# Performance work log

Hardware: AMD Instinct MI355X
Metric: run time of the kernel (lower is better)

The kernel has to match this reference:

```python
import jax, jax.numpy as jnp
import numpy as np

B, S, H, NH = 2, 2048, 2048, 16
DH = H // NH


def setup_inputs() -> dict:
    key = jax.random.key(0)
    ks = jax.random.split(key, 9)
    scale = 1.0 / np.sqrt(H)
    inp = {
        "hidden_state": jax.random.normal(ks[0], (B, S, H), dtype=jnp.float32),
        "Wq": jax.random.normal(ks[1], (H, H), dtype=jnp.float32) * scale,
        "bq": jnp.zeros((H,), dtype=jnp.float32),
        "Wk": jax.random.normal(ks[2], (H, H), dtype=jnp.float32) * scale,
        "bk": jnp.zeros((H,), dtype=jnp.float32),
        "Wv": jax.random.normal(ks[3], (H, H), dtype=jnp.float32) * scale,
        "bv": jnp.zeros((H,), dtype=jnp.float32),
        "Wo": jax.random.normal(ks[4], (H, H), dtype=jnp.float32) * scale,
        "bo": jnp.zeros((H,), dtype=jnp.float32),
    }
    # additive causal mask: 0 on/below diagonal, large negative above
    neg = jnp.float32(-1e9)
    tri = jnp.tril(jnp.ones((S, S), dtype=bool))
    inp["causal_mask"] = jnp.where(tri, 0.0, neg)[None, None, :, :]
    return inp


def reference(hidden_state, Wq, bq, Wk, bk, Wv, bv, Wo, bo, causal_mask):
    def split_heads(x):  # [B,S,H] -> [B,NH,S,DH]
        return x.reshape(B, S, NH, DH).transpose(0, 2, 1, 3)

    q = split_heads(hidden_state @ Wq + bq)
    k = split_heads(hidden_state @ Wk + bk)
    v = split_heads(hidden_state @ Wv + bv)

    scores = jnp.einsum("bhqd,bhkd->bhqk", q, k) / jnp.sqrt(jnp.float32(DH))
    scores = scores + causal_mask
    probs = jax.nn.softmax(scores, axis=-1)
    out = jnp.einsum("bhqk,bhkd->bhqd", probs, v)  # [B,NH,S,DH]
    out = out.transpose(0, 2, 1, 3).reshape(B, S, H)
    return out @ Wo + bo
```

## Files before the change

kernel.cpp:

```cpp
#include <hip/hip_runtime.h>
#include <cstdint>

typedef __attribute__((ext_vector_type(4))) float f32x4;
typedef __attribute__((ext_vector_type(16))) float f32x16;
typedef __attribute__((ext_vector_type(8))) __bf16 bf16x8;
typedef __attribute__((ext_vector_type(4))) unsigned short u16x4;
typedef __attribute__((ext_vector_type(2))) unsigned int u32x2;
typedef __attribute__((ext_vector_type(4))) float fvec4;

#define DEV __device__ __forceinline__
#define MFMA16(a, b, c) __builtin_amdgcn_mfma_f32_16x16x32_bf16((a), (b), (c), 0, 0, 0)
#define MFMA32(a, b, c) __builtin_amdgcn_mfma_f32_32x32x16_bf16((a), (b), (c), 0, 0, 0)

DEV unsigned short f2bf(float f) {
  union { float f; uint32_t u; } c; c.f = f;
  uint32_t u = c.u;
  return (unsigned short)((u + 0x7FFFu + ((u >> 16) & 1u)) >> 16);
}

DEV unsigned int pack2(float lo, float hi) {
  union { float f; uint32_t u; } a, b;
  a.f = lo; b.f = hi;
  return __builtin_amdgcn_perm(b.u + 0x8000u, a.u + 0x8000u, 0x07060302u);
}

DEV void gll16(const void* g, void* l) {
  __builtin_amdgcn_global_load_lds(
      (const __attribute__((address_space(1))) void*)(uintptr_t)g,
      (__attribute__((address_space(3))) void*)(uint32_t)(uintptr_t)l,
      16, 0, 0);
}

__global__ void cvt_bf16(const float* __restrict__ src, unsigned short* __restrict__ dst) {
  int i = (blockIdx.x * 256 + threadIdx.x) * 4;
  fvec4 v = *(const fvec4*)(src + i);
  u16x4 o;
  o[0] = f2bf(v[0]); o[1] = f2bf(v[1]); o[2] = f2bf(v[2]); o[3] = f2bf(v[3]);
  *(u16x4*)(dst + i) = o;
}

__global__ void transpose_cvt4(const float* __restrict__ W0, const float* __restrict__ W1,
                               const float* __restrict__ W2, const float* __restrict__ W3,
                               unsigned short* __restrict__ Dqkv, unsigned short* __restrict__ Do) {
  __shared__ float t[32][33];
  const float* W = blockIdx.z == 0 ? W0 : blockIdx.z == 1 ? W1 : blockIdx.z == 2 ? W2 : W3;
  unsigned short* WT = blockIdx.z < 3 ? Dqkv + (size_t)blockIdx.z * 2048 * 2048 : Do;
  int n0 = blockIdx.x * 32, k0 = blockIdx.y * 32;
  int x = threadIdx.x, y = threadIdx.y;
  #pragma unroll
  for (int i = 0; i < 32; i += 8)
    t[y + i][x] = W[(size_t)(k0 + y + i) * 2048 + n0 + x];
  __syncthreads();
  #pragma unroll
  for (int i = 0; i < 32; i += 8)
    WT[(size_t)(n0 + y + i) * 2048 + k0 + x] = f2bf(t[x][y + i]);
}

constexpr float QSC = 0.08838834764831845f * 1.4426950408889634f;

template <int MODE>
__global__ __launch_bounds__(256, 2) void gemm128(
    const unsigned short* __restrict__ A,
    const unsigned short* __restrict__ Bt,
    const float* __restrict__ b0, const float* __restrict__ b1,
    const float* __restrict__ b2,
    void* __restrict__ o0, void* __restrict__ o1, void* __restrict__ o2) {
  __shared__ unsigned short As[128 * 64];
  __shared__ unsigned short Bs[128 * 64];
  const int id = blockIdx.x;
  const int m0 = (((id & 7) << 2) | ((id >> 3) & 3)) * 128;
  const int n0 = (id >> 5) * 128;
  const int tid = threadIdx.x;
  const int wave = tid >> 6, lid = tid & 63;
  const int l16 = lid & 15, lq = lid >> 4;
  const int wm = (wave >> 1) * 64, wn = (wave & 1) * 64;

  const int srow = lid >> 3;
  const int sgrp = (lid & 7) ^ srow;

  f32x4 acc[4][4] = {};

  for (int k0 = 0; k0 < 2048; k0 += 64) {
    #pragma unroll
    for (int i = 0; i < 4; ++i) {
      const int t = wave * 4 + i;
      const int r = t * 8 + srow;
      gll16(A + (size_t)(m0 + r) * 2048 + k0 + sgrp * 8, (char*)As + t * 1024 + lid * 16);
      gll16(Bt + (size_t)(n0 + r) * 2048 + k0 + sgrp * 8, (char*)Bs + t * 1024 + lid * 16);
    }
    __syncthreads();
    #pragma unroll
    for (int kk = 0; kk < 2; ++kk) {
      const int G = kk * 4 + lq;
      bf16x8 af[4], bfr[4];
      #pragma unroll
      for (int i = 0; i < 4; ++i)
        af[i] = *(const bf16x8*)(As + (wm + i * 16 + l16) * 64 + ((G ^ (l16 & 7)) << 3));
      #pragma unroll
      for (int j = 0; j < 4; ++j)
        bfr[j] = *(const bf16x8*)(Bs + (wn + j * 16 + l16) * 64 + ((G ^ (l16 & 7)) << 3));
      #pragma unroll
      for (int i = 0; i < 4; ++i)
        #pragma unroll
        for (int j = 0; j < 4; ++j)
          acc[i][j] = MFMA16(af[i], bfr[j], acc[i][j]);
    }
    __syncthreads();
  }

  #pragma unroll
  for (int j = 0; j < 4; ++j) {
    const int c = n0 + wn + j * 16 + l16;
    if (MODE == 1) {
      const int which = c >> 11;
      const int hd = c & 2047;
      const int h = hd >> 7, d = hd & 127;
      const float* bp = which == 0 ? b0 : which == 1 ? b1 : b2;
      const float bv = bp[hd];
      if (which == 2) {
        #pragma unroll
        for (int i = 0; i < 4; ++i) {
          const int row0 = m0 + wm + i * 16 + lq * 4;
          const int bb = row0 >> 11, s0 = row0 & 2047;
          u16x4 pv;
          #pragma unroll
          for (int r = 0; r < 4; ++r) pv[r] = f2bf(acc[i][j][r] + bv);
          *(u16x4*)((unsigned short*)o2 + ((size_t)((bb * 16 + h) * 128 + d)) * 2048 + s0) = pv;
        }
      } else {
        const float sc = which == 0 ? QSC : 1.0f;
        unsigned short* op = which == 0 ? (unsigned short*)o0 : (unsigned short*)o1;
        #pragma unroll
        for (int i = 0; i < 4; ++i) {
          #pragma unroll
          for (int r = 0; r < 4; ++r) {
            const int row = m0 + wm + i * 16 + lq * 4 + r;
            const int bb = row >> 11, s = row & 2047;
            op[(size_t)((bb * 16 + h) * 2048 + s) * 128 + d] = f2bf((acc[i][j][r] + bv) * sc);
          }
        }
      }
    } else {
      const float bv = b0[c];
      #pragma unroll
      for (int i = 0; i < 4; ++i)
        #pragma unroll
        for (int r = 0; r < 4; ++r) {
          const int row = m0 + wm + i * 16 + lq * 4 + r;
          ((float*)o0)[(size_t)row * 2048 + c] = acc[i][j][r] + bv;
        }
    }
  }
}

__global__ __launch_bounds__(256, 2) void attn(
    const unsigned short* __restrict__ Q,
    const unsigned short* __restrict__ K,
    const unsigned short* __restrict__ Vt,
    unsigned short* __restrict__ ctx) {
  __shared__ unsigned short Ks[64 * 128];
  __shared__ unsigned short Vts[128 * 64];
  __shared__ unsigned short Ps[4 * 32 * 64];

  const int bh = blockIdx.y;
  const int jq = (bh < 16) ? (15 - (int)blockIdx.x) : (int)blockIdx.x;
  const int q0 = jq * 128;
  const int b = bh >> 4, h = bh & 15;
  const unsigned short* Qh = Q + (size_t)bh * 2048 * 128;
  const unsigned short* Kh = K + (size_t)bh * 2048 * 128;
  const unsigned short* Vth = Vt + (size_t)bh * 128 * 2048;

  const int tid = threadIdx.x;
  const int wave = tid >> 6, lid = tid & 63;
  const int l32 = lid & 31, half = lid >> 5;
  const int qrow = q0 + wave * 32 + l32;
  unsigned short* Pw = Ps + wave * 2048 + l32 * 64;
  const int qsw = l32 & 7;

  bf16x8 qf[8];
  #pragma unroll
  for (int ds = 0; ds < 8; ++ds)
    qf[ds] = *(const bf16x8*)(Qh + (size_t)qrow * 128 + ds * 16 + half * 8);

  float m_i = -1e30f, l_i = 0.f;
  f32x16 acc[4] = {};

  const int ntiles = 2 * jq + 2;
  for (int jt = 0; jt < ntiles; ++jt) {
    const int k0 = jt * 64;
    #pragma unroll
    for (int ii = 0; ii < 4; ++ii) {
      const int t = wave * 4 + ii;
      const int r = t * 4 + (lid >> 4);
      const int g = (lid & 15) ^ (r & 15);
      gll16(Kh + (size_t)(k0 + r) * 128 + g * 8, (char*)Ks + t * 1024 + lid * 16);
    }
    #pragma unroll
    for (int ii = 0; ii < 4; ++ii) {
      const int t = wave * 4 + ii;
      const int d = t * 8 + (lid >> 3);
      const int g = (lid & 7) ^ (d & 7);
      gll16(Vth + (size_t)d * 2048 + k0 + g * 8, (char*)Vts + t * 1024 + lid * 16);
    }
    __syncthreads();

    f32x16 sacc[2] = {};
    #pragma unroll
    for (int ds = 0; ds < 8; ++ds) {
      #pragma unroll
      for (int mb = 0; mb < 2; ++mb) {
        const int kr = mb * 32 + l32;
        bf16x8 af = *(const bf16x8*)(Ks + kr * 128 + (((ds * 2 + half) ^ (kr & 15)) << 3));
        sacc[mb] = MFMA32(af, qf[ds], sacc[mb]);
      }
    }

    if (jt >= 2 * jq) {
      #pragma unroll
      for (int mb = 0; mb < 2; ++mb)
        #pragma unroll
        for (int i = 0; i < 16; ++i) {
          const int kg = k0 + mb * 32 + (i & 3) + 8 * (i >> 2) + 4 * half;
          if (kg > qrow) sacc[mb][i] = -1e30f;
        }
    }

    float tmax = -1e30f;
    #pragma unroll
    for (int mb = 0; mb < 2; ++mb)
      #pragma unroll
      for (int i = 0; i < 16; ++i) tmax = fmaxf(tmax, sacc[mb][i]);
    tmax = fmaxf(tmax, __shfl_xor(tmax, 32));

    const float mnew = fmaxf(m_i, tmax);
    const float alpha = exp2f(m_i - mnew);
    m_i = mnew;

    float ps = 0.f;
    #pragma unroll
    for (int mb = 0; mb < 2; ++mb) {
      #pragma unroll
      for (int i = 0; i < 16; ++i) {
        sacc[mb][i] = exp2f(sacc[mb][i] - mnew);
        ps += sacc[mb][i];
      }
      #pragma unroll
      for (int u = 0; u < 4; ++u) {
        u32x2 w;
        w[0] = pack2(sacc[mb][4 * u], sacc[mb][4 * u + 1]);
        w[1] = pack2(sacc[mb][4 * u + 2], sacc[mb][4 * u + 3]);
        *(u32x2*)(Pw + (((u + mb * 4) ^ qsw) << 3) + half * 4) = w;
      }
    }
    ps += __shfl_xor(ps, 32);
    l_i = l_i * alpha + ps;
    #pragma unroll
    for (int db = 0; db < 4; ++db)
      #pragma unroll
      for (int i = 0; i < 16; ++i) acc[db][i] *= alpha;

    #pragma unroll
    for (int ks = 0; ks < 4; ++ks) {
      bf16x8 pf = *(const bf16x8*)(Pw + (((ks * 2 + half) ^ qsw) << 3));
      #pragma unroll
      for (int db = 0; db < 4; ++db) {
        const int d = db * 32 + l32;
        bf16x8 vf = *(const bf16x8*)(Vts + d * 64 + (((ks * 2 + half) ^ (d & 7)) << 3));
        acc[db] = MFMA32(vf, pf, acc[db]);
      }
    }
    __syncthreads();
  }

  const float inv = 1.f / l_i;
  const size_t base = ((size_t)(b * 2048 + qrow)) * 2048 + h * 128;
  #pragma unroll
  for (int db = 0; db < 4; ++db) {
    #pragma unroll
    for (int u = 0; u < 4; ++u) {
      u32x2 w;
      w[0] = pack2(acc[db][4 * u] * inv, acc[db][4 * u + 1] * inv);
      w[1] = pack2(acc[db][4 * u + 2] * inv, acc[db][4 * u + 3] * inv);
      *(u32x2*)(ctx + base + db * 32 + 8 * u + 4 * half) = w;
    }
  }
}

extern "C" void kernel_launch(void* const* d_in, const int* in_sizes, int n_in,
                              void* d_out, int out_size, void* d_ws, size_t ws_size,
                              hipStream_t stream) {
  const float* hs = (const float*)d_in[0];
  const float* Wq = (const float*)d_in[1];
  const float* bq = (const float*)d_in[2];
  const float* Wk = (const float*)d_in[3];
  const float* bk = (const float*)d_in[4];
  const float* Wv = (const float*)d_in[5];
  const float* bv = (const float*)d_in[6];
  const float* Wo = (const float*)d_in[7];
  const float* bo = (const float*)d_in[8];
  float* out = (float*)d_out;

  char* ws = (char*)d_ws;
  unsigned short* hsb   = (unsigned short*)(ws);
  unsigned short* wqkvt = (unsigned short*)(ws + (16 << 20));
  unsigned short* wot   = (unsigned short*)(ws + (40 << 20));
  unsigned short* Qb    = (unsigned short*)(ws + (48 << 20));
  unsigned short* Kb    = (unsigned short*)(ws + (64 << 20));
  unsigned short* Vtb   = (unsigned short*)(ws + (80 << 20));
  unsigned short* ctx   = (unsigned short*)(ws + (96 << 20));

  cvt_bf16<<<dim3(8192), dim3(256), 0, stream>>>(hs, hsb);
  transpose_cvt4<<<dim3(64, 64, 4), dim3(32, 8), 0, stream>>>(Wq, Wk, Wv, Wo, wqkvt, wot);

  gemm128<1><<<dim3(1536), 256, 0, stream>>>(hsb, wqkvt, bq, bk, bv,
                                             (void*)Qb, (void*)Kb, (void*)Vtb);
  attn<<<dim3(16, 32), 256, 0, stream>>>(Qb, Kb, Vtb, ctx);
  gemm128<0><<<dim3(512), 256, 0, stream>>>(ctx, wot, bo, nullptr, nullptr,
                                            (void*)out, nullptr, nullptr);
}
```

Before: 392.3 us.

## Replace QKV projection GEMM with 256x256-tile, 8-wave pipelined kernel

The fused QKV projection now runs in a new kernel that computes 256x256 output tiles with 512 threads. It double-buffers LDS through direct global-to-LDS loads, interleaved across eight sub-phases per pair of K-steps. The kernel uses explicit barriers, waitcnt, sched_barrier and setprio around MFMA clusters, and an XCD-aware block remap. The aim is to raise arithmetic intensity and overlap memory with compute, at the cost of heavy register and LDS use (128 KB shared). The old gemm128 mode-1 epilogue is removed, leaving the template serving only the output projection.

```diff
diff --git a/kernel.cpp b/kernel.cpp
--- a/kernel.cpp
+++ b/kernel.cpp
@@ -111,43 +111,139 @@
   #pragma unroll
   for (int j = 0; j < 4; ++j) {
     const int c = n0 + wn + j * 16 + l16;
-    if (MODE == 1) {
-      const int which = c >> 11;
-      const int hd = c & 2047;
-      const int h = hd >> 7, d = hd & 127;
-      const float* bp = which == 0 ? b0 : which == 1 ? b1 : b2;
-      const float bv = bp[hd];
-      if (which == 2) {
+    const float bv = b0[c];
+    #pragma unroll
+    for (int i = 0; i < 4; ++i)
+      #pragma unroll
+      for (int r = 0; r < 4; ++r) {
+        const int row = m0 + wm + i * 16 + lq * 4 + r;
+        ((float*)o0)[(size_t)row * 2048 + c] = acc[i][j][r] + bv;
+      }
+  }
+}
+
+#define STA(c, kt, q) do { \
+  _Pragma("unroll") for (int jj = 0; jj < 2; ++jj) { \
+    const int j = (q) + jj * 2; \
+    const int r = j * 64 + srow; \
+    const int g = schk ^ (r & 7); \
+    gll16(A + (size_t)(m0 + r) * 2048 + ((kt) << 6) + g * 8, \
+          (char*)Als + (c) * 32768 + j * 8192 + tid * 16); \
+  } } while (0)
+
+#define STB(c, kt, q) do { \
+  _Pragma("unroll") for (int jj = 0; jj < 2; ++jj) { \
+    const int j = (q) * 2 + jj; \
+    const int L = j * 64 + srow; \
+    const int n = (((L & 127) >> 5) << 6) + ((L >> 7) << 5) + (L & 31); \
+    const int g = schk ^ (L & 7); \
+    gll16(Bt + (size_t)(n0 + n) * 2048 + ((kt) << 6) + g * 8, \
+          (char*)Bls + (c) * 32768 + j * 8192 + tid * 16); \
+  } } while (0)
+
+#define PHASE(CUR, QM, QN, STAGE, VM) do { \
+  bf16x8 af[4][2], bf_[2][2]; \
+  const unsigned short* Ab = Als + (CUR) * 16384; \
+  const unsigned short* Bb = Bls + (CUR) * 16384; \
+  _Pragma("unroll") for (int m = 0; m < 4; ++m) { \
+    const int row = wr * 128 + ((QM) * 4 + m) * 16 + l16; \
+    _Pragma("unroll") for (int kk = 0; kk < 2; ++kk) \
+      af[m][kk] = *(const bf16x8*)(Ab + row * 64 + (((kk * 4 + lq) ^ (row & 7)) << 3)); \
+  } \
+  _Pragma("unroll") for (int n = 0; n < 2; ++n) { \
+    const int bg = wc * 64 + ((QN) * 2 + n) * 16 + l16; \
+    const int L = (((bg >> 5) & 1) << 7) | ((bg >> 6) << 5) | (bg & 31); \
+    _Pragma("unroll") for (int kk = 0; kk < 2; ++kk) \
+      bf_[n][kk] = *(const bf16x8*)(Bb + L * 64 + (((kk * 4 + lq) ^ (L & 7)) << 3)); \
+  } \
+  STAGE; \
+  __builtin_amdgcn_sched_barrier(0); \
+  __builtin_amdgcn_s_barrier(); \
+  asm volatile("s_waitcnt lgkmcnt(0)" ::: "memory"); \
+  __builtin_amdgcn_sched_barrier(0); \
+  __builtin_amdgcn_s_setprio(1); \
+  _Pragma("unroll") for (int m = 0; m < 4; ++m) \
+    _Pragma("unroll") for (int n = 0; n < 2; ++n) \
+      _Pragma("unroll") for (int kk = 0; kk < 2; ++kk) \
+        acc[(QM) * 4 + m][(QN) * 2 + n] = \
+            MFMA16(af[m][kk], bf_[n][kk], acc[(QM) * 4 + m][(QN) * 2 + n]); \
+  __builtin_amdgcn_s_setprio(0); \
+  __builtin_amdgcn_sched_barrier(0); \
+  VM; \
+  __builtin_amdgcn_s_barrier(); \
+} while (0)
+
+__global__ __launch_bounds__(512, 2) void gemm256qkv(
+    const unsigned short* __restrict__ A,
+    const unsigned short* __restrict__ Bt,
+    const float* __restrict__ b0, const float* __restrict__ b1,
+    const float* __restrict__ b2,
+    unsigned short* __restrict__ oQ, unsigned short* __restrict__ oK,
+    unsigned short* __restrict__ oV) {
+  __shared__ unsigned short Als[32768];
+  __shared__ unsigned short Bls[32768];
+
+  const int id = blockIdx.x;
+  const int wg = (id & 7) * 48 + (id >> 3);
+  const int mt = wg / 24, nt = wg % 24;
+  const int m0 = mt << 8, n0 = nt << 8;
+
+  const int tid = threadIdx.x;
+  const int wave = tid >> 6, lid = tid & 63;
+  const int l16 = lid & 15, lq = lid >> 4;
+  const int wr = wave >> 2, wc = wave & 3;
+  const int srow = tid >> 3;
+  const int schk = tid & 7;
+
+  f32x4 acc[8][4] = {};
+
+  STA(0, 0, 0); STA(0, 0, 1); STB(0, 0, 0); STB(0, 0, 1);
+  STA(1, 1, 0); STB(1, 1, 0);
+  asm volatile("s_waitcnt vmcnt(4)" ::: "memory");
+  __builtin_amdgcn_s_barrier();
+
+  #pragma unroll 1
+  for (int i = 0; i < 16; ++i) {
+    const int t1 = 2 * i + 1;
+    const int t2 = (2 * i + 2 < 32) ? 2 * i + 2 : 31;
+    const int t3 = (2 * i + 3 < 32) ? 2 * i + 3 : 31;
+    PHASE(0, 0, 0, { STA(1, t1, 1); STB(1, t1, 1); }, );
+    PHASE(0, 0, 1, , );
+    PHASE(0, 1, 0, STA(0, t2, 0), );
+    PHASE(0, 1, 1, STB(0, t2, 0), asm volatile("s_waitcnt vmcnt(4)" ::: "memory"));
+    PHASE(1, 0, 0, { STA(0, t2, 1); STB(0, t2, 1); }, );
+    PHASE(1, 0, 1, , );
+    PHASE(1, 1, 0, STA(1, t3, 0), );
+    PHASE(1, 1, 1, STB(1, t3, 0), asm volatile("s_waitcnt vmcnt(4)" ::: "memory"));
+  }
+
+  const int which = n0 >> 11;
+  const float* bp = which == 0 ? b0 : which == 1 ? b1 : b2;
+  #pragma unroll
+  for (int n = 0; n < 4; ++n) {
+    const int hd = (n0 & 2047) + wc * 64 + n * 16 + l16;
+    const int h = hd >> 7, d = hd & 127;
+    const float bv = bp[hd];
+    if (which == 2) {
+      #pragma unroll
+      for (int m = 0; m < 8; ++m) {
+        const int row0 = m0 + wr * 128 + m * 16 + lq * 4;
+        const int bb = row0 >> 11, s0 = row0 & 2047;
+        u16x4 pv;
         #pragma unroll
-        for (int i = 0; i < 4; ++i) {
-          const int row0 = m0 + wm + i * 16 + lq * 4;
-          const int bb = row0 >> 11, s0 = row0 & 2047;
-          u16x4 pv;
-          #pragma unroll
-          for (int r = 0; r < 4; ++r) pv[r] = f2bf(acc[i][j][r] + bv);
-          *(u16x4*)((unsigned short*)o2 + ((size_t)((bb * 16 + h) * 128 + d)) * 2048 + s0) = pv;
-        }
-      } else {
-        const float sc = which == 0 ? QSC : 1.0f;
-        unsigned short* op = which == 0 ? (unsigned short*)o0 : (unsigned short*)o1;
-        #pragma unroll
-        for (int i = 0; i < 4; ++i) {
-          #pragma unroll
-          for (int r = 0; r < 4; ++r) {
-            const int row = m0 + wm + i * 16 + lq * 4 + r;
-            const int bb = row >> 11, s = row & 2047;
-            op[(size_t)((bb * 16 + h) * 2048 + s) * 128 + d] = f2bf((acc[i][j][r] + bv) * sc);
-          }
-        }
+        for (int r = 0; r < 4; ++r) pv[r] = f2bf(acc[m][n][r] + bv);
+        *(u16x4*)(oV + ((size_t)((bb * 16 + h) * 128 + d)) * 2048 + s0) = pv;
       }
     } else {
-      const float bv = b0[c];
-      #pragma unroll
-      for (int i = 0; i < 4; ++i)
+      const float sc = which == 0 ? QSC : 1.0f;
+      unsigned short* op = which == 0 ? oQ : oK;
+      #pragma unroll
+      for (int m = 0; m < 8; ++m)
         #pragma unroll
         for (int r = 0; r < 4; ++r) {
-          const int row = m0 + wm + i * 16 + lq * 4 + r;
-          ((float*)o0)[(size_t)row * 2048 + c] = acc[i][j][r] + bv;
+          const int row = m0 + wr * 128 + m * 16 + lq * 4 + r;
+          const int bb = row >> 11, s = row & 2047;
+          op[(size_t)((bb * 16 + h) * 2048 + s) * 128 + d] = f2bf((acc[m][n][r] + bv) * sc);
         }
     }
   }
@@ -312,8 +408,7 @@
   cvt_bf16<<<dim3(8192), dim3(256), 0, stream>>>(hs, hsb);
   transpose_cvt4<<<dim3(64, 64, 4), dim3(32, 8), 0, stream>>>(Wq, Wk, Wv, Wo, wqkvt, wot);
 
-  gemm128<1><<<dim3(1536), 256, 0, stream>>>(hsb, wqkvt, bq, bk, bv,
-                                             (void*)Qb, (void*)Kb, (void*)Vtb);
+  gemm256qkv<<<dim3(384), dim3(512), 0, stream>>>(hsb, wqkvt, bq, bk, bv, Qb, Kb, Vtb);
   attn<<<dim3(16, 32), 256, 0, stream>>>(Qb, Kb, Vtb, ctx);
   gemm128<0><<<dim3(512), 256, 0, stream>>>(ctx, wot, bo, nullptr, nullptr,
                                             (void*)out, nullptr, nullptr);
```

Result: slower. 413.3 us (+5.4%).

## Add dedicated pipelined 128x256 QKV projection GEMM with XCD-aware tile mapping

Applied to the files above, without the earlier changes.

Replaces the generic 128x128 QKV projection GEMM with a dedicated 512-thread kernel using 128x256 tiles. It double-buffers LDS with direct global-to-LDS loads, interleaves loads with MFMA phases under explicit barriers, waitcnts and setprio, and maps blocks so each XCD covers a fixed set of N tiles for L2 reuse. The goal is to hide memory latency and raise MFMA utilisation in the largest GEMM. The hand-scheduled waits and barriers add complexity, and any miscount would be a correctness risk.

```diff
diff --git a/kernel.cpp b/kernel.cpp
--- a/kernel.cpp
+++ b/kernel.cpp
@@ -111,46 +111,150 @@
   #pragma unroll
   for (int j = 0; j < 4; ++j) {
     const int c = n0 + wn + j * 16 + l16;
-    if (MODE == 1) {
-      const int which = c >> 11;
-      const int hd = c & 2047;
-      const int h = hd >> 7, d = hd & 127;
-      const float* bp = which == 0 ? b0 : which == 1 ? b1 : b2;
-      const float bv = bp[hd];
-      if (which == 2) {
+    const float bv = b0[c];
+    #pragma unroll
+    for (int i = 0; i < 4; ++i)
+      #pragma unroll
+      for (int r = 0; r < 4; ++r) {
+        const int row = m0 + wm + i * 16 + lq * 4 + r;
+        ((float*)o0)[(size_t)row * 2048 + c] = acc[i][j][r] + bv;
+      }
+  }
+}
+
+__global__ __launch_bounds__(512, 2) void gemmqkv(
+    const unsigned short* __restrict__ A,
+    const unsigned short* __restrict__ Bt,
+    const float* __restrict__ b0, const float* __restrict__ b1,
+    const float* __restrict__ b2,
+    unsigned short* __restrict__ oQ, unsigned short* __restrict__ oK,
+    unsigned short* __restrict__ oV) {
+  __shared__ unsigned short Als[2 * 128 * 64];
+  __shared__ unsigned short Bls[2 * 256 * 64];
+
+  const int id = blockIdx.x;
+  const int xcd = id & 7, loc = id >> 3;
+  const int mt = loc & 31, ntl = loc >> 5;
+  const int nt = xcd * 3 + ntl;
+  const int m0 = mt << 7, n0 = nt << 8;
+
+  const int tid = threadIdx.x;
+  const int wave = tid >> 6, lid = tid & 63;
+  const int l16 = lid & 15, lq = lid >> 4;
+  const int wr = wave >> 2, wc = wave & 3;
+  const int srow = tid >> 3;
+  const int g8 = ((tid & 7) ^ (srow & 7)) * 8;
+
+  f32x4 acc[4][4] = {};
+  bf16x8 aq[2][2], bq[4][2];
+
+#define STA_(c, kt) do { \
+    _Pragma("unroll") for (int u = 0; u < 2; ++u) \
+      gll16(A + (size_t)(m0 + u * 64 + srow) * 2048 + ((kt) << 6) + g8, \
+            (char*)Als + (c) * 16384 + u * 8192 + tid * 16); \
+  } while (0)
+
+#define STB_(c, kt) do { \
+    _Pragma("unroll") for (int u = 0; u < 4; ++u) \
+      gll16(Bt + (size_t)(n0 + u * 64 + srow) * 2048 + ((kt) << 6) + g8, \
+            (char*)Bls + (c) * 32768 + u * 8192 + tid * 16); \
+  } while (0)
+
+#define RDA_(c, h) do { \
+    _Pragma("unroll") for (int m = 0; m < 2; ++m) { \
+      const int row = wr * 64 + ((h) * 2 + m) * 16 + l16; \
+      _Pragma("unroll") for (int kk = 0; kk < 2; ++kk) \
+        aq[m][kk] = *(const bf16x8*)(Als + (c) * 8192 + row * 64 + \
+                                     (((kk * 4 + lq) ^ (row & 7)) << 3)); \
+    } } while (0)
+
+#define RDB_(c) do { \
+    _Pragma("unroll") for (int n = 0; n < 4; ++n) { \
+      const int bg = wc * 64 + n * 16 + l16; \
+      _Pragma("unroll") for (int kk = 0; kk < 2; ++kk) \
+        bq[n][kk] = *(const bf16x8*)(Bls + (c) * 16384 + bg * 64 + \
+                                     (((kk * 4 + lq) ^ (bg & 7)) << 3)); \
+    } } while (0)
+
+#define MM_(h) do { \
+    _Pragma("unroll") for (int m = 0; m < 2; ++m) \
+      _Pragma("unroll") for (int n = 0; n < 4; ++n) \
+        _Pragma("unroll") for (int kk = 0; kk < 2; ++kk) \
+          acc[(h) * 2 + m][n] = MFMA16(aq[m][kk], bq[n][kk], acc[(h) * 2 + m][n]); \
+  } while (0)
+
+#define SB_ __builtin_amdgcn_sched_barrier(0)
+#define BAR_ __builtin_amdgcn_s_barrier()
+#define LGKM_ asm volatile("s_waitcnt lgkmcnt(0)" ::: "memory")
+#define VM4_ asm volatile("s_waitcnt vmcnt(4)" ::: "memory")
+
+  STB_(0, 0); STA_(0, 0); STB_(1, 1);
+  VM4_;
+  BAR_;
+
+  #pragma unroll 1
+  for (int i = 0; i < 16; ++i) {
+    const int t1 = 2 * i + 1;
+    const int t2 = (2 * i + 2 < 32) ? 2 * i + 2 : 31;
+    const int t3 = (2 * i + 3 < 32) ? 2 * i + 3 : 31;
+    RDA_(0, 0); RDB_(0); STA_(1, t1);
+    SB_; BAR_; LGKM_; SB_;
+    __builtin_amdgcn_s_setprio(1); MM_(0); __builtin_amdgcn_s_setprio(0);
+    SB_; BAR_;
+    RDA_(0, 1); STB_(0, t2);
+    SB_; BAR_; LGKM_; SB_;
+    __builtin_amdgcn_s_setprio(1); MM_(1); __builtin_amdgcn_s_setprio(0);
+    SB_; VM4_; BAR_;
+    RDA_(1, 0); RDB_(1); STA_(0, t2);
+    SB_; BAR_; LGKM_; SB_;
+    __builtin_amdgcn_s_setprio(1); MM_(0); __builtin_amdgcn_s_setprio(0);
+    SB_; BAR_;
+    RDA_(1, 1); STB_(1, t3);
+    SB_; BAR_; LGKM_; SB_;
+    __builtin_amdgcn_s_setprio(1); MM_(1); __builtin_amdgcn_s_setprio(0);
+    SB_; VM4_; BAR_;
+  }
+  asm volatile("s_waitcnt vmcnt(0)" ::: "memory");
+
+  const int which = n0 >> 11;
+  const float* bp = which == 0 ? b0 : which == 1 ? b1 : b2;
+  #pragma unroll
+  for (int n = 0; n < 4; ++n) {
+    const int hd = (n0 & 2047) + wc * 64 + n * 16 + l16;
+    const int h = hd >> 7, d = hd & 127;
+    const float bv = bp[hd];
+    if (which == 2) {
+      #pragma unroll
+      for (int m = 0; m < 4; ++m) {
+        const int row0 = m0 + wr * 64 + m * 16 + lq * 4;
+        const int bb = row0 >> 11, s0 = row0 & 2047;
+        u16x4 pv;
         #pragma unroll
-        for (int i = 0; i < 4; ++i) {
-          const int row0 = m0 + wm + i * 16 + lq * 4;
-          const int bb = row0 >> 11, s0 = row0 & 2047;
-          u16x4 pv;
-          #pragma unroll
-          for (int r = 0; r < 4; ++r) pv[r] = f2bf(acc[i][j][r] + bv);
-          *(u16x4*)((unsigned short*)o2 + ((size_t)((bb * 16 + h) * 128 + d)) * 2048 + s0) = pv;
-        }
-      } else {
-        const float sc = which == 0 ? QSC : 1.0f;
-        unsigned short* op = which == 0 ? (unsigned short*)o0 : (unsigned short*)o1;
-        #pragma unroll
-        for (int i = 0; i < 4; ++i) {
-          #pragma unroll
-          for (int r = 0; r < 4; ++r) {
-            const int row = m0 + wm + i * 16 + lq * 4 + r;
-            const int bb = row >> 11, s = row & 2047;
-            op[(size_t)((bb * 16 + h) * 2048 + s) * 128 + d] = f2bf((acc[i][j][r] + bv) * sc);
-          }
-        }
+        for (int r = 0; r < 4; ++r) pv[r] = f2bf(acc[m][n][r] + bv);
+        *(u16x4*)(oV + ((size_t)((bb * 16 + h) * 128 + d)) * 2048 + s0) = pv;
       }
     } else {
-      const float bv = b0[c];
-      #pragma unroll
-      for (int i = 0; i < 4; ++i)
+      const float sc = which == 0 ? QSC : 1.0f;
+      unsigned short* op = which == 0 ? oQ : oK;
+      #pragma unroll
+      for (int m = 0; m < 4; ++m)
         #pragma unroll
         for (int r = 0; r < 4; ++r) {
-          const int row = m0 + wm + i * 16 + lq * 4 + r;
-          ((float*)o0)[(size_t)row * 2048 + c] = acc[i][j][r] + bv;
+          const int row = m0 + wr * 64 + m * 16 + lq * 4 + r;
+          const int bb = row >> 11, s = row & 2047;
+          op[(size_t)((bb * 16 + h) * 2048 + s) * 128 + d] = f2bf((acc[m][n][r] + bv) * sc);
         }
     }
   }
+#undef STA_
+#undef STB_
+#undef RDA_
+#undef RDB_
+#undef MM_
+#undef SB_
+#undef BAR_
+#undef LGKM_
+#undef VM4_
 }
 
 __global__ __launch_bounds__(256, 2) void attn(
@@ -312,8 +416,7 @@
   cvt_bf16<<<dim3(8192), dim3(256), 0, stream>>>(hs, hsb);
   transpose_cvt4<<<dim3(64, 64, 4), dim3(32, 8), 0, stream>>>(Wq, Wk, Wv, Wo, wqkvt, wot);
 
-  gemm128<1><<<dim3(1536), 256, 0, stream>>>(hsb, wqkvt, bq, bk, bv,
-                                             (void*)Qb, (void*)Kb, (void*)Vtb);
+  gemmqkv<<<dim3(768), dim3(512), 0, stream>>>(hsb, wqkvt, bq, bk, bv, Qb, Kb, Vtb);
   attn<<<dim3(16, 32), 256, 0, stream>>>(Qb, Kb, Vtb, ctx);
   gemm128<0><<<dim3(512), 256, 0, stream>>>(ctx, wot, bo, nullptr, nullptr,
                                             (void*)out, nullptr, nullptr);
```

Measured after the change: 389.0 us. About the same (-0.8%).
